# Performance work log

Hardware: AMD Instinct MI355X
Metric: run time of the kernel (lower is better)

Reference implementation:

```python
import jax, jax.numpy as jnp
import numpy as np

H = 512
IN = 64
OUT = 1


def _lstm_layer(x, W_ih, W_hh, b_ih, b_hh):
    # x: (B, T, D). PyTorch gate order: i, f, g, o stacked along 4H.
    B, T, _ = x.shape
    Hd = W_hh.shape[1]
    # Precompute input contribution for all timesteps (one big GEMM).
    xg = jnp.einsum('btd,gd->btg', x, W_ih) + b_ih + b_hh  # (B, T, 4H)

    def step(carry, xg_t):
        h, c = carry
        gates = xg_t + h @ W_hh.T  # (B, 4H)
        i, f, g, o = jnp.split(gates, 4, axis=-1)
        i = jax.nn.sigmoid(i)
        f = jax.nn.sigmoid(f)
        g = jnp.tanh(g)
        o = jax.nn.sigmoid(o)
        c = f * c + i * g
        h = o * jnp.tanh(c)
        return (h, c), h

    h0 = jnp.zeros((B, Hd), x.dtype)
    c0 = jnp.zeros((B, Hd), x.dtype)
    (_, _), hs = jax.lax.scan(step, (h0, c0), jnp.swapaxes(xg, 0, 1))
    return jnp.swapaxes(hs, 0, 1)  # (B, T, H)


def setup_inputs() -> dict:
    key = jax.random.key(0)
    ks = jax.random.split(key, 12)
    s = 1.0 / np.sqrt(H)  # PyTorch LSTM init scale
    u = lambda k, shp: jax.random.uniform(k, shp, jnp.float32, -s, s)
    return {
        'x': jax.random.normal(ks[0], (64, 512, IN), jnp.float32),
        'W_ih0': u(ks[1], (4 * H, IN)),
        'W_hh0': u(ks[2], (4 * H, H)),
        'b_ih0': u(ks[3], (4 * H,)),
        'b_hh0': u(ks[4], (4 * H,)),
        'W_ih1': u(ks[5], (4 * H, H)),
        'W_hh1': u(ks[6], (4 * H, H)),
        'b_ih1': u(ks[7], (4 * H,)),
        'b_hh1': u(ks[8], (4 * H,)),
        'fc_w': u(ks[9], (OUT, H)),
        'fc_b': u(ks[10], (OUT,)),
    }


def reference(x, W_ih0, W_hh0, b_ih0, b_hh0, W_ih1, W_hh1, b_ih1, b_hh1, fc_w, fc_b):
    # Two stacked LSTM layers (eval mode: inter-layer dropout disabled),
    # then linear head on the last timestep's hidden state.
    h1 = _lstm_layer(x, W_ih0, W_hh0, b_ih0, b_hh0)   # (B, T, H)
    h2 = _lstm_layer(h1, W_ih1, W_hh1, b_ih1, b_hh1)  # (B, T, H)
    return h2[:, -1, :] @ fc_w.T + fc_b               # (B, OUT)
```

## Files before the change

### kernel.cpp

```cpp
#include <hip/hip_runtime.h>
#include <stdint.h>

static constexpr int NBLK = 256;
static constexpr int NTHR = 256;
static constexpr int Hd   = 512;
static constexpr int Td   = 512;
static constexpr int IND  = 64;
static constexpr int Bd   = 64;
static constexpr int HBUF = Bd * Hd;
static constexpr int HR   = 520;
static constexpr unsigned POIS32 = 0xAAAAAAAAu;

typedef __attribute__((ext_vector_type(8))) short short8;
typedef __attribute__((ext_vector_type(4))) float f4;

#define MFMA(a, b, c) __builtin_amdgcn_mfma_f32_16x16x32_bf16((a), (b), (c), 0, 0, 0)

__device__ __forceinline__ uint64_t ld_agent64(const uint64_t* p) {
  return __hip_atomic_load((uint64_t*)p, __ATOMIC_RELAXED, __HIP_MEMORY_SCOPE_AGENT);
}
__device__ __forceinline__ void st_agent32(unsigned* p, unsigned v) {
  __hip_atomic_store(p, v, __ATOMIC_RELAXED, __HIP_MEMORY_SCOPE_AGENT);
}
__device__ __forceinline__ float sigmoidf_(float v) { return 1.0f / (1.0f + __expf(-v)); }
__device__ __forceinline__ float tanhf_(float v) {
  v = fminf(15.0f, fmaxf(-15.0f, v));
  float e = __expf(2.0f * v);
  return (e - 1.0f) / (e + 1.0f);
}
__device__ __forceinline__ unsigned short bf16_rne(float f) {
  unsigned u = __float_as_uint(f);
  unsigned r = u + 0x7FFFu + ((u >> 16) & 1u);
  return (unsigned short)(r >> 16);
}
__device__ __forceinline__ unsigned pack_h(float h) {
  unsigned short hb = bf16_rne(h);
  float hf = __uint_as_float((unsigned)hb << 16);
  unsigned short lb = bf16_rne(h - hf);
  unsigned pk = ((unsigned)hb << 16) | (unsigned)lb;
  if (pk == POIS32) pk ^= 1u;
  return pk;
}
__device__ __forceinline__ int good64(uint64_t w) {
  return (int)((unsigned)w != POIS32) & (int)((unsigned)(w >> 32) != POIS32);
}
__device__ __forceinline__ void poll16(const uint64_t* base, int tid, uint64_t* tmp) {
  const uint64_t* p15 = base + 15 * 256 + tid;
  int guard = 0;
  for (;;) {
    uint64_t w = ld_agent64(p15);
    if (good64(w) || ++guard > (1 << 18)) break;
    __builtin_amdgcn_s_sleep(1);
  }
  guard = 0;
  for (;;) {
    unsigned ok = 1;
    #pragma unroll
    for (int k = 0; k < 16; ++k) tmp[k] = ld_agent64(base + k * 256 + tid);
    #pragma unroll
    for (int k = 0; k < 16; ++k) ok &= (unsigned)good64(tmp[k]);
    if (ok || ++guard > (1 << 16)) break;
  }
}

__global__ __launch_bounds__(256) void split_x_kernel(
    const float* __restrict__ x, short* __restrict__ xhi, short* __restrict__ xlo) {
  int i = blockIdx.x * 256 + threadIdx.x;
  float4 v = ((const float4*)x)[i];
  float f[4] = {v.x, v.y, v.z, v.w};
  unsigned h[4], l[4];
  #pragma unroll
  for (int e = 0; e < 4; ++e) {
    unsigned short hb = bf16_rne(f[e]);
    float r = f[e] - __uint_as_float((unsigned)hb << 16);
    h[e] = hb; l[e] = bf16_rne(r);
  }
  uint2 hp = {h[0] | (h[1] << 16), h[2] | (h[3] << 16)};
  uint2 lp = {l[0] | (l[1] << 16), l[2] | (l[3] << 16)};
  *(uint2*)&xhi[i * 4] = hp;
  *(uint2*)&xlo[i * 4] = lp;
}

__global__ __launch_bounds__(NTHR, 1) void lstm2_flow(
    const float* __restrict__ Wih0, const float* __restrict__ Whh0,
    const float* __restrict__ bih0, const float* __restrict__ bhh0,
    const float* __restrict__ Wih1, const float* __restrict__ Whh1,
    const float* __restrict__ bih1, const float* __restrict__ bhh1,
    const float* __restrict__ fcw,  const float* __restrict__ fcb,
    float* __restrict__ out,
    const short* __restrict__ xhi, const short* __restrict__ xlo,
    unsigned* __restrict__ h1, unsigned* __restrict__ h2)
{
  __shared__ short hiA1[16 * HR];
  __shared__ short loA1[16 * HR];
  __shared__ short hiA2[16 * HR];
  __shared__ short loA2[16 * HR];
  __shared__ short Blo[4 * 16 * 64 * 8];
  __shared__ float g_lds[4][16][16];
  __shared__ float red[NTHR];

  const int tid  = threadIdx.x;
  const int wave = tid >> 6;
  const int lane = tid & 63;
  const int nB   = lane & 15;
  const int q    = lane >> 4;
  const int mA   = lane & 15;

  const int xcd   = blockIdx.x & 7;
  const int layer = xcd >> 2;
  const int mt    = xcd & 3;
  const int jt    = blockIdx.x >> 3;
  const int jBase = jt * 16;
  const int bBase = mt * 16;
  const int wrow  = wave * Hd + jBase + nB;

  const int pm = tid >> 4;
  const int pn = tid & 15;

  if (layer == 0) {
    short8 bh[18], bl[18];
    {
      const float* Wh = Whh0 + (size_t)wrow * Hd;
      const float* Wi = Wih0 + (size_t)wrow * IND;
      #pragma unroll
      for (int kt = 0; kt < 18; ++kt) {
        const float* src = (kt < 16) ? (Wh + kt * 32 + q * 8) : (Wi + (kt - 16) * 32 + q * 8);
        float wv[8];
        *(float4*)&wv[0] = *(const float4*)src;
        *(float4*)&wv[4] = *(const float4*)(src + 4);
        #pragma unroll
        for (int j = 0; j < 8; ++j) {
          unsigned short hb = bf16_rne(wv[j]);
          float r = wv[j] - __uint_as_float((unsigned)hb << 16);
          ((short*)&bh[kt])[j] = (short)hb;
          ((short*)&bl[kt])[j] = (short)bf16_rne(r);
        }
      }
    }
    float bias[4];
    #pragma unroll
    for (int g4 = 0; g4 < 4; ++g4) {
      int r = g4 * Hd + jBase + pn;
      bias[g4] = bih0[r] + bhh0[r];
    }
    float c1 = 0.0f;

    for (int t = 0; t < Td; ++t) {
      f4 a0 = {0.f,0.f,0.f,0.f}, a1 = {0.f,0.f,0.f,0.f}, a2 = {0.f,0.f,0.f,0.f};
      f4 d0 = {0.f,0.f,0.f,0.f}, d1 = {0.f,0.f,0.f,0.f}, d2 = {0.f,0.f,0.f,0.f};
      {
        const size_t xb = ((size_t)(bBase + mA) * Td + t) * IND;
        short8 x0h = *(const short8*)&xhi[xb + q * 8];
        short8 x0l = *(const short8*)&xlo[xb + q * 8];
        short8 x1h = *(const short8*)&xhi[xb + 32 + q * 8];
        short8 x1l = *(const short8*)&xlo[xb + 32 + q * 8];
        a0 = MFMA(x0h, bh[16], a0); a1 = MFMA(x0h, bl[16], a1); a2 = MFMA(x0l, bh[16], a2);
        d0 = MFMA(x1h, bh[17], d0); d1 = MFMA(x1h, bl[17], d1); d2 = MFMA(x1l, bh[17], d2);
      }
      if (t >= 1) {
        const uint64_t* s1 = (const uint64_t*)(h1 + (size_t)(t - 1) * HBUF) + bBase * 256;
        uint64_t tmp[16];
        poll16(s1, tid, tmp);
        #pragma unroll
        for (int k = 0; k < 16; ++k) {
          unsigned p0 = (unsigned)tmp[k], p1 = (unsigned)(tmp[k] >> 32);
          *(unsigned*)&hiA1[k * HR + tid * 2] = __builtin_amdgcn_perm(p1, p0, 0x07060302u);
          *(unsigned*)&loA1[k * HR + tid * 2] = __builtin_amdgcn_perm(p1, p0, 0x05040100u);
        }
      }
      __syncthreads();

      if (t >= 1) {
        #pragma unroll
        for (int kt = 0; kt < 16; kt += 2) {
          short8 ah0 = *(const short8*)&hiA1[mA * HR + kt * 32 + q * 8];
          short8 al0 = *(const short8*)&loA1[mA * HR + kt * 32 + q * 8];
          short8 ah1 = *(const short8*)&hiA1[mA * HR + (kt + 1) * 32 + q * 8];
          short8 al1 = *(const short8*)&loA1[mA * HR + (kt + 1) * 32 + q * 8];
          a0 = MFMA(ah0, bh[kt], a0);
          d0 = MFMA(ah1, bh[kt + 1], d0);
          a1 = MFMA(ah0, bl[kt], a1);
          d1 = MFMA(ah1, bl[kt + 1], d1);
          a2 = MFMA(al0, bh[kt], a2);
          d2 = MFMA(al1, bh[kt + 1], d2);
        }
      }
      #pragma unroll
      for (int r2 = 0; r2 < 4; ++r2)
        g_lds[wave][q * 4 + r2][nB] =
            (a0[r2] + d0[r2]) + (a1[r2] + d1[r2]) + (a2[r2] + d2[r2]);
      __syncthreads();

      {
        float pi = g_lds[0][pm][pn] + bias[0];
        float pf = g_lds[1][pm][pn] + bias[1];
        float pg = g_lds[2][pm][pn] + bias[2];
        float po = g_lds[3][pm][pn] + bias[3];
        float ig = sigmoidf_(pi), fg = sigmoidf_(pf), gg = tanhf_(pg), og = sigmoidf_(po);
        c1 = fmaf(fg, c1, ig * gg);
        float h = og * tanhf_(c1);
        st_agent32(h1 + (size_t)t * HBUF + (bBase + pm) * Hd + jBase + pn, pack_h(h));
      }
    }

    if (blockIdx.x == 0) {
      const int b = tid >> 2, q4 = tid & 3;
      float sum = 0.0f;
      #pragma unroll
      for (int ch = 0; ch < 4; ++ch) {
        const uint64_t* hp = (const uint64_t*)(h2 + (size_t)(Td - 1) * HBUF) + b * 256 + q4 * 64 + ch * 16;
        uint64_t w[16];
        int guard = 0;
        for (;;) {
          unsigned ok = 1;
          #pragma unroll
          for (int u = 0; u < 16; ++u) w[u] = ld_agent64(hp + u);
          #pragma unroll
          for (int u = 0; u < 16; ++u) ok &= (unsigned)good64(w[u]);
          if (ok || ++guard > (1 << 17)) break;
          __builtin_amdgcn_s_sleep(1);
        }
        #pragma unroll
        for (int u = 0; u < 16; ++u) {
          int cw = q4 * 64 + ch * 16 + u;
          unsigned plo = (unsigned)w[u], phi = (unsigned)(w[u] >> 32);
          float vlo = __uint_as_float(plo & 0xFFFF0000u) + __uint_as_float(plo << 16);
          float vhi = __uint_as_float(phi & 0xFFFF0000u) + __uint_as_float(phi << 16);
          sum = fmaf(vlo, fcw[2 * cw], fmaf(vhi, fcw[2 * cw + 1], sum));
        }
      }
      red[tid] = sum;
      __syncthreads();
      if (q4 == 0) out[b] = red[tid] + red[tid + 1] + red[tid + 2] + red[tid + 3] + fcb[0];
    }
  } else {
    short8 bh[32], bl[16];
    {
      const float* Wi = Wih1 + (size_t)wrow * Hd;
      const float* Wh = Whh1 + (size_t)wrow * Hd;
      #pragma unroll
      for (int kt = 0; kt < 16; ++kt) {
        float wv[8];
        *(float4*)&wv[0] = *(const float4*)(Wi + kt * 32 + q * 8);
        *(float4*)&wv[4] = *(const float4*)(Wi + kt * 32 + q * 8 + 4);
        #pragma unroll
        for (int j = 0; j < 8; ++j) {
          unsigned short hb = bf16_rne(wv[j]);
          float r = wv[j] - __uint_as_float((unsigned)hb << 16);
          ((short*)&bh[kt])[j] = (short)hb;
          ((short*)&bl[kt])[j] = (short)bf16_rne(r);
        }
      }
      #pragma unroll
      for (int kt = 0; kt < 16; ++kt) {
        float wv[8];
        *(float4*)&wv[0] = *(const float4*)(Wh + kt * 32 + q * 8);
        *(float4*)&wv[4] = *(const float4*)(Wh + kt * 32 + q * 8 + 4);
        short lo8[8];
        #pragma unroll
        for (int j = 0; j < 8; ++j) {
          unsigned short hb = bf16_rne(wv[j]);
          float r = wv[j] - __uint_as_float((unsigned)hb << 16);
          ((short*)&bh[16 + kt])[j] = (short)hb;
          lo8[j] = (short)bf16_rne(r);
        }
        *(short8*)&Blo[((wave * 16 + kt) * 64 + lane) * 8] = *(short8*)lo8;
      }
    }
    float bias[4];
    #pragma unroll
    for (int g4 = 0; g4 < 4; ++g4) {
      int r = g4 * Hd + jBase + pn;
      bias[g4] = bih1[r] + bhh1[r];
    }
    float c2 = 0.0f;
    __syncthreads();

    for (int t = 0; t < Td; ++t) {
      const uint64_t* s1 = (const uint64_t*)(h1 + (size_t)t * HBUF) + bBase * 256;
      if (t >= 1) {
        const uint64_t* s2 = (const uint64_t*)(h2 + (size_t)(t - 1) * HBUF) + bBase * 256;
        uint64_t t1[16], t2[16];
        {
          const uint64_t* p1 = s1 + 15 * 256 + tid;
          const uint64_t* p2 = s2 + 15 * 256 + tid;
          int guard = 0;
          for (;;) {
            uint64_t w1 = ld_agent64(p1);
            uint64_t w2 = ld_agent64(p2);
            if ((good64(w1) & good64(w2)) != 0) break;
            if (++guard > (1 << 18)) break;
            __builtin_amdgcn_s_sleep(1);
          }
        }
        int guard = 0;
        for (;;) {
          unsigned ok = 1;
          #pragma unroll
          for (int k = 0; k < 16; ++k) {
            t1[k] = ld_agent64(s1 + k * 256 + tid);
            t2[k] = ld_agent64(s2 + k * 256 + tid);
          }
          #pragma unroll
          for (int k = 0; k < 16; ++k) ok &= (unsigned)(good64(t1[k]) & good64(t2[k]));
          if (ok || ++guard > (1 << 16)) break;
        }
        #pragma unroll
        for (int k = 0; k < 16; ++k) {
          unsigned p0 = (unsigned)t1[k], p1 = (unsigned)(t1[k] >> 32);
          *(unsigned*)&hiA1[k * HR + tid * 2] = __builtin_amdgcn_perm(p1, p0, 0x07060302u);
          *(unsigned*)&loA1[k * HR + tid * 2] = __builtin_amdgcn_perm(p1, p0, 0x05040100u);
          unsigned q0 = (unsigned)t2[k], q1 = (unsigned)(t2[k] >> 32);
          *(unsigned*)&hiA2[k * HR + tid * 2] = __builtin_amdgcn_perm(q1, q0, 0x07060302u);
          *(unsigned*)&loA2[k * HR + tid * 2] = __builtin_amdgcn_perm(q1, q0, 0x05040100u);
        }
      } else {
        uint64_t t1[16];
        poll16(s1, tid, t1);
        #pragma unroll
        for (int k = 0; k < 16; ++k) {
          unsigned p0 = (unsigned)t1[k], p1 = (unsigned)(t1[k] >> 32);
          *(unsigned*)&hiA1[k * HR + tid * 2] = __builtin_amdgcn_perm(p1, p0, 0x07060302u);
          *(unsigned*)&loA1[k * HR + tid * 2] = __builtin_amdgcn_perm(p1, p0, 0x05040100u);
        }
      }
      __syncthreads();

      f4 a0 = {0.f,0.f,0.f,0.f}, a1 = {0.f,0.f,0.f,0.f}, a2 = {0.f,0.f,0.f,0.f};
      f4 d0 = {0.f,0.f,0.f,0.f}, d1 = {0.f,0.f,0.f,0.f}, d2 = {0.f,0.f,0.f,0.f};
      #pragma unroll
      for (int kt = 0; kt < 16; kt += 2) {
        short8 ah0 = *(const short8*)&hiA1[mA * HR + kt * 32 + q * 8];
        short8 al0 = *(const short8*)&loA1[mA * HR + kt * 32 + q * 8];
        short8 ah1 = *(const short8*)&hiA1[mA * HR + (kt + 1) * 32 + q * 8];
        short8 al1 = *(const short8*)&loA1[mA * HR + (kt + 1) * 32 + q * 8];
        a0 = MFMA(ah0, bh[kt], a0);
        d0 = MFMA(ah1, bh[kt + 1], d0);
        a1 = MFMA(ah0, bl[kt], a1);
        d1 = MFMA(ah1, bl[kt + 1], d1);
        a2 = MFMA(al0, bh[kt], a2);
        d2 = MFMA(al1, bh[kt + 1], d2);
      }
      if (t >= 1) {
        #pragma unroll
        for (int kt = 0; kt < 16; kt += 2) {
          short8 ah0  = *(const short8*)&hiA2[mA * HR + kt * 32 + q * 8];
          short8 al0  = *(const short8*)&loA2[mA * HR + kt * 32 + q * 8];
          short8 wlo0 = *(const short8*)&Blo[((wave * 16 + kt) * 64 + lane) * 8];
          short8 ah1  = *(const short8*)&hiA2[mA * HR + (kt + 1) * 32 + q * 8];
          short8 al1  = *(const short8*)&loA2[mA * HR + (kt + 1) * 32 + q * 8];
          short8 wlo1 = *(const short8*)&Blo[((wave * 16 + kt + 1) * 64 + lane) * 8];
          a0 = MFMA(ah0, bh[16 + kt], a0);
          d0 = MFMA(ah1, bh[16 + kt + 1], d0);
          a1 = MFMA(ah0, wlo0, a1);
          d1 = MFMA(ah1, wlo1, d1);
          a2 = MFMA(al0, bh[16 + kt], a2);
          d2 = MFMA(al1, bh[16 + kt + 1], d2);
        }
      }
      #pragma unroll
      for (int r2 = 0; r2 < 4; ++r2)
        g_lds[wave][q * 4 + r2][nB] =
            (a0[r2] + d0[r2]) + (a1[r2] + d1[r2]) + (a2[r2] + d2[r2]);
      __syncthreads();

      {
        float pi = g_lds[0][pm][pn] + bias[0];
        float pf = g_lds[1][pm][pn] + bias[1];
        float pg = g_lds[2][pm][pn] + bias[2];
        float po = g_lds[3][pm][pn] + bias[3];
        float ig = sigmoidf_(pi), fg = sigmoidf_(pf), gg = tanhf_(pg), og = sigmoidf_(po);
        c2 = fmaf(fg, c2, ig * gg);
        float h = og * tanhf_(c2);
        st_agent32(h2 + (size_t)t * HBUF + (bBase + pm) * Hd + jBase + pn, pack_h(h));
      }
    }
  }
}

extern "C" void kernel_launch(void* const* d_in, const int* in_sizes, int n_in,
                              void* d_out, int out_size, void* d_ws, size_t ws_size,
                              hipStream_t stream) {
  const float* x    = (const float*)d_in[0];
  const float* Wih0 = (const float*)d_in[1];
  const float* Whh0 = (const float*)d_in[2];
  const float* bih0 = (const float*)d_in[3];
  const float* bhh0 = (const float*)d_in[4];
  const float* Wih1 = (const float*)d_in[5];
  const float* Whh1 = (const float*)d_in[6];
  const float* bih1 = (const float*)d_in[7];
  const float* bhh1 = (const float*)d_in[8];
  const float* fcw  = (const float*)d_in[9];
  const float* fcb  = (const float*)d_in[10];

  char* base = (char*)d_ws;
  short* xhi = (short*)base;
  const size_t xplane = (size_t)Bd * Td * IND;
  short* xlo = xhi + xplane;
  unsigned* h1 = (unsigned*)(xlo + xplane);
  unsigned* h2 = h1 + (size_t)Td * HBUF;

  const size_t need = 4 * xplane + 2 * (size_t)Td * HBUF * 4;
  if (ws_size < need) return;

  hipLaunchKernelGGL(split_x_kernel, dim3((unsigned)(xplane / 4 / 256)), dim3(256), 0, stream,
                     x, xhi, xlo);
  hipLaunchKernelGGL(lstm2_flow, dim3(NBLK), dim3(NTHR), 0, stream,
                     Wih0, Whh0, bih0, bhh0, Wih1, Whh1, bih1, bhh1, fcw, fcb,
                     (float*)d_out, xhi, xlo, h1, h2);
}
```

Before: 2.413 ms.

## Issue sentinel loads early and split layer-2 polling to overlap with MFMA

Sentinel loads for the previous-step hidden-state buffers are issued at the top of each timestep, before the input-contribution MFMAs, so their latency overlaps compute. In the layer-2 loop, polling of h1 and h2 is split. The h1 contribution is computed first, then the loop waits for the h2 recurrence from the previous step and adds an extra __syncthreads before the recurrent MFMAs. This moves the critical-path h2 wait later, at the cost of an additional block barrier per step.

```diff
diff --git a/kernel.cpp b/kernel.cpp
--- a/kernel.cpp
+++ b/kernel.cpp
@@ -44,13 +44,15 @@
 __device__ __forceinline__ int good64(uint64_t w) {
   return (int)((unsigned)w != POIS32) & (int)((unsigned)(w >> 32) != POIS32);
 }
-__device__ __forceinline__ void poll16(const uint64_t* base, int tid, uint64_t* tmp) {
+__device__ __forceinline__ void poll16_from(const uint64_t* base, int tid, uint64_t w0,
+                                            uint64_t* tmp) {
   const uint64_t* p15 = base + 15 * 256 + tid;
+  uint64_t w = w0;
   int guard = 0;
-  for (;;) {
-    uint64_t w = ld_agent64(p15);
-    if (good64(w) || ++guard > (1 << 18)) break;
+  while (!good64(w)) {
+    if (++guard > (1 << 18)) break;
     __builtin_amdgcn_s_sleep(1);
+    w = ld_agent64(p15);
   }
   guard = 0;
   for (;;) {
@@ -61,6 +63,9 @@
     for (int k = 0; k < 16; ++k) ok &= (unsigned)good64(tmp[k]);
     if (ok || ++guard > (1 << 16)) break;
   }
+}
+__device__ __forceinline__ void poll16(const uint64_t* base, int tid, uint64_t* tmp) {
+  poll16_from(base, tid, ld_agent64(base + 15 * 256 + tid), tmp);
 }
 
 __global__ __launch_bounds__(256) void split_x_kernel(
@@ -146,6 +151,11 @@
     float c1 = 0.0f;
 
     for (int t = 0; t < Td; ++t) {
+      const uint64_t* s1 = (t >= 1)
+          ? (const uint64_t*)(h1 + (size_t)(t - 1) * HBUF) + bBase * 256 : (const uint64_t*)0;
+      uint64_t sent1 = 0;
+      if (t >= 1) sent1 = ld_agent64(s1 + 15 * 256 + tid);
+
       f4 a0 = {0.f,0.f,0.f,0.f}, a1 = {0.f,0.f,0.f,0.f}, a2 = {0.f,0.f,0.f,0.f};
       f4 d0 = {0.f,0.f,0.f,0.f}, d1 = {0.f,0.f,0.f,0.f}, d2 = {0.f,0.f,0.f,0.f};
       {
@@ -158,9 +168,8 @@
         d0 = MFMA(x1h, bh[17], d0); d1 = MFMA(x1h, bl[17], d1); d2 = MFMA(x1l, bh[17], d2);
       }
       if (t >= 1) {
-        const uint64_t* s1 = (const uint64_t*)(h1 + (size_t)(t - 1) * HBUF) + bBase * 256;
         uint64_t tmp[16];
-        poll16(s1, tid, tmp);
+        poll16_from(s1, tid, sent1, tmp);
         #pragma unroll
         for (int k = 0; k < 16; ++k) {
           unsigned p0 = (unsigned)tmp[k], p1 = (unsigned)(tmp[k] >> 32);
@@ -278,45 +287,16 @@
 
     for (int t = 0; t < Td; ++t) {
       const uint64_t* s1 = (const uint64_t*)(h1 + (size_t)t * HBUF) + bBase * 256;
-      if (t >= 1) {
-        const uint64_t* s2 = (const uint64_t*)(h2 + (size_t)(t - 1) * HBUF) + bBase * 256;
-        uint64_t t1[16], t2[16];
-        {
-          const uint64_t* p1 = s1 + 15 * 256 + tid;
-          const uint64_t* p2 = s2 + 15 * 256 + tid;
-          int guard = 0;
-          for (;;) {
-            uint64_t w1 = ld_agent64(p1);
-            uint64_t w2 = ld_agent64(p2);
-            if ((good64(w1) & good64(w2)) != 0) break;
-            if (++guard > (1 << 18)) break;
-            __builtin_amdgcn_s_sleep(1);
-          }
-        }
-        int guard = 0;
-        for (;;) {
-          unsigned ok = 1;
-          #pragma unroll
-          for (int k = 0; k < 16; ++k) {
-            t1[k] = ld_agent64(s1 + k * 256 + tid);
-            t2[k] = ld_agent64(s2 + k * 256 + tid);
-          }
-          #pragma unroll
-          for (int k = 0; k < 16; ++k) ok &= (unsigned)(good64(t1[k]) & good64(t2[k]));
-          if (ok || ++guard > (1 << 16)) break;
-        }
-        #pragma unroll
-        for (int k = 0; k < 16; ++k) {
-          unsigned p0 = (unsigned)t1[k], p1 = (unsigned)(t1[k] >> 32);
-          *(unsigned*)&hiA1[k * HR + tid * 2] = __builtin_amdgcn_perm(p1, p0, 0x07060302u);
-          *(unsigned*)&loA1[k * HR + tid * 2] = __builtin_amdgcn_perm(p1, p0, 0x05040100u);
-          unsigned q0 = (unsigned)t2[k], q1 = (unsigned)(t2[k] >> 32);
-          *(unsigned*)&hiA2[k * HR + tid * 2] = __builtin_amdgcn_perm(q1, q0, 0x07060302u);
-          *(unsigned*)&loA2[k * HR + tid * 2] = __builtin_amdgcn_perm(q1, q0, 0x05040100u);
-        }
-      } else {
+      const uint64_t* s2 = (t >= 1)
+          ? (const uint64_t*)(h2 + (size_t)(t - 1) * HBUF) + bBase * 256 : (const uint64_t*)0;
+
+      uint64_t sent1 = ld_agent64(s1 + 15 * 256 + tid);
+      uint64_t sent2 = 0;
+      if (t >= 1) sent2 = ld_agent64(s2 + 15 * 256 + tid);
+
+      {
         uint64_t t1[16];
-        poll16(s1, tid, t1);
+        poll16_from(s1, tid, sent1, t1);
         #pragma unroll
         for (int k = 0; k < 16; ++k) {
           unsigned p0 = (unsigned)t1[k], p1 = (unsigned)(t1[k] >> 32);
@@ -341,6 +321,19 @@
         a2 = MFMA(al0, bh[kt], a2);
         d2 = MFMA(al1, bh[kt + 1], d2);
       }
+
+      if (t >= 1) {
+        uint64_t t2[16];
+        poll16_from(s2, tid, sent2, t2);
+        #pragma unroll
+        for (int k = 0; k < 16; ++k) {
+          unsigned q0 = (unsigned)t2[k], q1 = (unsigned)(t2[k] >> 32);
+          *(unsigned*)&hiA2[k * HR + tid * 2] = __builtin_amdgcn_perm(q1, q0, 0x07060302u);
+          *(unsigned*)&loA2[k * HR + tid * 2] = __builtin_amdgcn_perm(q1, q0, 0x05040100u);
+        }
+      }
+      __syncthreads();
+
       if (t >= 1) {
         #pragma unroll
         for (int kt = 0; kt < 16; kt += 2) {
```

New measurement: 2.380 ms. No clear change (-1.3%).
